# Optimization experiments

Hardware: AMD Instinct MI355X
Metric: run time of the kernel (lower is better)

The kernel has to match this reference:

```python
import jax, jax.numpy as jnp
import numpy as np

THETA0 = 3.0
THETA = 5.0
BIG = 1e10  # stands in for +inf in the squared-distance transform


def _edt_sq_1d(f):
    # f: [..., n] of squared distances; returns min_j (i-j)^2 + f[j] per i.
    n = f.shape[-1]
    i = jnp.arange(n, dtype=f.dtype)
    d2 = (i[:, None] - i[None, :]) ** 2  # [n, n]
    return jnp.min(f[..., None, :] + d2, axis=-1)


def _edt(mask):
    # Exact Euclidean distance from each voxel to the nearest zero of `mask`
    # (matches scipy.ndimage.distance_transform_edt on a binary mask),
    # via the separable squared-distance transform applied axis by axis.
    f = jnp.where(mask > 0.5, jnp.asarray(BIG, mask.dtype), jnp.asarray(0.0, mask.dtype))
    for ax in range(1, mask.ndim):  # skip batch axis 0
        f = jnp.moveaxis(_edt_sq_1d(jnp.moveaxis(f, ax, -1)), -1, ax)
    return jnp.sqrt(f)


def setup_inputs() -> dict:
    key = jax.random.key(0)
    k1, k2 = jax.random.split(key)
    B, D, H, W = 2, 64, 96, 96
    pred = jax.random.uniform(k1, (B, D, H, W), dtype=jnp.float32)  # probabilities
    target = jax.random.randint(k2, (B, D, H, W), 0, 2).astype(jnp.float32)  # binary mask
    return {"pred": pred, "target": target}


def reference(pred, target):
    # Signed distance phi = dist_to_foreground_boundary framework: 
    # dist_pos = EDT(target) (distance to nearest background voxel),
    # dist_neg = EDT(1 - target).
    dist_pos = _edt(target)
    dist_neg = _edt(1.0 - target)
    a = jnp.abs(dist_neg - dist_pos)
    w = jnp.where(
        a <= THETA0,
        1.0,
        jnp.where(a >= THETA, 0.0, 1.0 - (a - THETA0) / (THETA - THETA0)),
    )
    w = jax.lax.stop_gradient(w)  # original computes weights from detached numpy target

    # binary_cross_entropy with torch's log clamp at -100
    log_p = jnp.clip(jnp.log(pred), -100.0)
    log_1mp = jnp.clip(jnp.log(1.0 - pred), -100.0)
    bce = -(target * log_p + (1.0 - target) * log_1mp)  # [B, D, H, W]

    num = jnp.sum(bce * w, axis=(1, 2, 3))
    den = jnp.sum(w, axis=(1, 2, 3)) + 1e-5
    return jnp.mean(num / den)
```

## Files before the change

### kernel.cpp

```cpp
#include <hip/hip_runtime.h>
#include <math.h>

#define BDIM 2
#define DDIM 64
#define HDIM 96
#define WDIM 96
#define HW   (HDIM * WDIM)
#define DHW  (DDIM * HW)

#define DT 16
#define DH 24
#define HT 8
#define HH 16
#define WT 32
#define NROWS (DH * HH)
#define NBLK  (BDIM * (DDIM / DT) * (HDIM / HT) * (WDIM / WT))

__global__ void init_acc(float* __restrict__ acc) {
    if (threadIdx.x < 4) acc[threadIdx.x] = 0.0f;
    if (threadIdx.x == 4) ((int*)acc)[4] = 0;
}

__device__ __forceinline__ unsigned nearest2i(unsigned occ) {
    unsigned r = 25u;
    if (occ & 0x101u) r = 16u;
    if (occ & 0x082u) r = 9u;
    if (occ & 0x044u) r = 4u;
    if (occ & 0x028u) r = 1u;
    if (occ & 0x010u) r = 0u;
    return r;
}

__global__ __launch_bounds__(256) void boundary_fused(const float* __restrict__ pred,
                                                      const float* __restrict__ target,
                                                      float* __restrict__ acc,
                                                      float* __restrict__ out) {
    __shared__ unsigned fgb[NROWS * 2];
    __shared__ unsigned vbb[NROWS * 2];
    __shared__ unsigned char swp[DH * HH * WT];
    __shared__ unsigned char swn[DH * HH * WT];
    __shared__ unsigned char whp[DH * HT * WT];
    __shared__ unsigned char whn[DH * HT * WT];
    __shared__ float rsum[8];

    const int tid = threadIdx.x;
    int x = blockIdx.x;
    const int wt = x % 3;  x /= 3;
    const int ht = x % 12; x /= 12;
    const int dt = x % 4;
    const int b  = x / 4;
    const int d0 = dt * DT, h0 = ht * HT, w0 = wt * WT;

    for (int i = tid; i < NROWS * 2; i += 256) { fgb[i] = 0u; vbb[i] = 0u; }
    __syncthreads();

    for (int idx = tid; idx < NROWS * 10; idx += 256) {
        const int row = idx / 10, q = idx - row * 10;
        const int dr = row >> 4, hr = row & 15;
        const int d = d0 - 4 + dr, h = h0 - 4 + hr;
        if (d < 0 || d >= DDIM || h < 0 || h >= HDIM) continue;
        const int wbase = w0 - 4 + q * 4;
        const float* rowp = target + ((size_t)(b * DDIM + d) * HDIM + h) * WDIM;
        unsigned fgn = 0u, vn = 0u;
        if (wbase >= 0 && wbase <= WDIM - 4) {
            float4 v4 = *(const float4*)(rowp + wbase);
            fgn = (unsigned)(v4.x > 0.5f) | ((unsigned)(v4.y > 0.5f) << 1) |
                  ((unsigned)(v4.z > 0.5f) << 2) | ((unsigned)(v4.w > 0.5f) << 3);
            vn = 0xFu;
        } else {
            for (int j = 0; j < 4; ++j) {
                int w = wbase + j;
                if (w >= 0 && w < WDIM) {
                    vn |= 1u << j;
                    if (rowp[w] > 0.5f) fgn |= 1u << j;
                }
            }
        }
        if (vn) {
            const int k = q * 4, word = k >> 5, sh = k & 31;
            if (fgn) atomicOr(&fgb[row * 2 + word], fgn << sh);
            atomicOr(&vbb[row * 2 + word], vn << sh);
        }
    }
    __syncthreads();

    for (int idx = tid; idx < NROWS * WT; idx += 256) {
        const int row = idx >> 5, wi = idx & 31;
        unsigned long long fg = ((unsigned long long)fgb[row * 2 + 1] << 32) | fgb[row * 2];
        unsigned long long vv = ((unsigned long long)vbb[row * 2 + 1] << 32) | vbb[row * 2];
        unsigned of = (unsigned)(fg >> wi) & 0x1FFu;
        unsigned ov = (unsigned)(vv >> wi) & 0x1FFu;
        unsigned ob = ~of & ov;
        swn[idx] = (unsigned char)nearest2i(of);
        swp[idx] = (unsigned char)nearest2i(ob);
    }
    __syncthreads();

    for (int idx = tid; idx < DH * HT * WT; idx += 256) {
        const int dr = idx >> 8;
        const int hh = (idx >> 5) & 7;
        const int wi = idx & 31;
        unsigned p = 25u, n = 25u;
        #pragma unroll
        for (int t = 0; t < 9; ++t) {
            const unsigned d2 = (unsigned)((t - 4) * (t - 4));
            const int src = (dr * HH + hh + t) * WT + wi;
            p = min(p, d2 + (unsigned)swp[src]);
            n = min(n, d2 + (unsigned)swn[src]);
        }
        whp[idx] = (unsigned char)p;
        whn[idx] = (unsigned char)n;
    }
    __syncthreads();

    float num = 0.f, den = 0.f;
    #pragma unroll 4
    for (int it = 0; it < 16; ++it) {
        const int idx = tid + 256 * it;
        const int di = idx >> 8;
        const int hh = (idx >> 5) & 7;
        const int wi = idx & 31;
        unsigned p = 25u, n = 25u;
        #pragma unroll
        for (int t = 0; t < 9; ++t) {
            const unsigned d2 = (unsigned)((t - 4) * (t - 4));
            const int src = ((di + t) * HT + hh) * WT + wi;
            p = min(p, d2 + (unsigned)whp[src]);
            n = min(n, d2 + (unsigned)whn[src]);
        }
        const size_t g = ((size_t)(b * DDIM + d0 + di) * HDIM + h0 + hh) * WDIM + w0 + wi;
        const float pr = pred[g];
        const float tg = target[g];
        const float dp = sqrtf((float)p);
        const float dn = sqrtf((float)n);
        const float a  = fabsf(dn - dp);
        float w;
        if (a <= 3.0f)      w = 1.0f;
        else if (a >= 5.0f) w = 0.0f;
        else                w = 1.0f - (a - 3.0f) * 0.5f;
        const float lp  = fmaxf(logf(pr), -100.0f);
        const float l1  = fmaxf(logf(1.0f - pr), -100.0f);
        const float bce = -(tg * lp + (1.0f - tg) * l1);
        num += bce * w;
        den += w;
    }

    for (int off = 32; off > 0; off >>= 1) {
        num += __shfl_down(num, off);
        den += __shfl_down(den, off);
    }
    if ((tid & 63) == 0) {
        rsum[tid >> 6]       = num;
        rsum[4 + (tid >> 6)] = den;
    }
    __syncthreads();
    if (tid == 0) {
        float ns = rsum[0] + rsum[1] + rsum[2] + rsum[3];
        float ds = rsum[4] + rsum[5] + rsum[6] + rsum[7];
        atomicAdd(&acc[b], ns);
        atomicAdd(&acc[2 + b], ds);
        __threadfence();
        int done = atomicAdd((int*)acc + 4, 1);
        if (done == NBLK - 1) {
            __threadfence();
            float n0 = atomicAdd(&acc[0], 0.0f);
            float n1 = atomicAdd(&acc[1], 0.0f);
            float d0_ = atomicAdd(&acc[2], 0.0f);
            float d1_ = atomicAdd(&acc[3], 0.0f);
            out[0] = 0.5f * (n0 / (d0_ + 1e-5f) + n1 / (d1_ + 1e-5f));
        }
    }
}

extern "C" void kernel_launch(void* const* d_in, const int* in_sizes, int n_in,
                              void* d_out, int out_size, void* d_ws, size_t ws_size,
                              hipStream_t stream) {
    const float* pred   = (const float*)d_in[0];
    const float* target = (const float*)d_in[1];
    float* acc = (float*)d_ws;
    float* out = (float*)d_out;

    init_acc<<<1, 64, 0, stream>>>(acc);
    boundary_fused<<<NBLK, 256, 0, stream>>>(pred, target, acc, out);
}
```

Before: 95.13 us.

## Pack EDT distances four per word with SWAR min and ballot-based bitmask build

Halves the depth tile to 8 so each block holds 16 halo rows, which doubles the number of blocks. Foreground bitmasks are built with a wave ballot over 40 lanes instead of shared atomicOr. Squared distances for four voxels are packed as bytes in one 32-bit word, and the H and D passes use a SWAR byte-wise min, which cuts shared-memory traffic and ALU work. The final stage loads pred and target as float4. The smaller depth tile raises the halo overhead ratio from 24/16 to 16/8, and the byte packing depends on every value staying below 128.

```diff
diff --git a/kernel.cpp b/kernel.cpp
--- a/kernel.cpp
+++ b/kernel.cpp
@@ -8,11 +8,11 @@
 #define HW   (HDIM * WDIM)
 #define DHW  (DDIM * HW)
 
-#define DT 16
-#define DH 24
+#define DT 8
 #define HT 8
+#define WT 32
+#define DH 16
 #define HH 16
-#define WT 32
 #define NROWS (DH * HH)
 #define NBLK  (BDIM * (DDIM / DT) * (HDIM / HT) * (WDIM / WT))
 
@@ -31,118 +31,139 @@
     return r;
 }
 
+__device__ __forceinline__ unsigned vminu4(unsigned a, unsigned b) {
+    unsigned c = ((a | 0x80808080u) - b) & 0x80808080u;
+    unsigned m = (c - (c >> 7)) | c;
+    return a ^ ((a ^ b) & m);
+}
+
 __global__ __launch_bounds__(256) void boundary_fused(const float* __restrict__ pred,
                                                       const float* __restrict__ target,
                                                       float* __restrict__ acc,
                                                       float* __restrict__ out) {
-    __shared__ unsigned fgb[NROWS * 2];
-    __shared__ unsigned vbb[NROWS * 2];
-    __shared__ unsigned char swp[DH * HH * WT];
-    __shared__ unsigned char swn[DH * HH * WT];
-    __shared__ unsigned char whp[DH * HT * WT];
-    __shared__ unsigned char whn[DH * HT * WT];
+    __shared__ unsigned long long fgb[NROWS];
+    __shared__ unsigned swp[NROWS * 8];
+    __shared__ unsigned swn[NROWS * 8];
+    __shared__ unsigned whp[DH * HT * 8];
+    __shared__ unsigned whn[DH * HT * 8];
     __shared__ float rsum[8];
 
     const int tid = threadIdx.x;
     int x = blockIdx.x;
     const int wt = x % 3;  x /= 3;
     const int ht = x % 12; x /= 12;
-    const int dt = x % 4;
-    const int b  = x / 4;
+    const int dt = x % 8;
+    const int b  = x / 8;
     const int d0 = dt * DT, h0 = ht * HT, w0 = wt * WT;
 
-    for (int i = tid; i < NROWS * 2; i += 256) { fgb[i] = 0u; vbb[i] = 0u; }
-    __syncthreads();
-
-    for (int idx = tid; idx < NROWS * 10; idx += 256) {
-        const int row = idx / 10, q = idx - row * 10;
-        const int dr = row >> 4, hr = row & 15;
-        const int d = d0 - 4 + dr, h = h0 - 4 + hr;
-        if (d < 0 || d >= DDIM || h < 0 || h >= HDIM) continue;
-        const int wbase = w0 - 4 + q * 4;
-        const float* rowp = target + ((size_t)(b * DDIM + d) * HDIM + h) * WDIM;
-        unsigned fgn = 0u, vn = 0u;
-        if (wbase >= 0 && wbase <= WDIM - 4) {
-            float4 v4 = *(const float4*)(rowp + wbase);
-            fgn = (unsigned)(v4.x > 0.5f) | ((unsigned)(v4.y > 0.5f) << 1) |
-                  ((unsigned)(v4.z > 0.5f) << 2) | ((unsigned)(v4.w > 0.5f) << 3);
-            vn = 0xFu;
-        } else {
+    unsigned long long vb_row = (1ULL << 40) - 1;
+    if (wt == 0) vb_row &= ~0xFULL;
+    if (wt == 2) vb_row &= (1ULL << 36) - 1;
+
+    {
+        const int lane = tid & 63;
+        const int wv   = tid >> 6;
+        #pragma unroll 4
+        for (int i = 0; i < 64; ++i) {
+            const int row = wv * 64 + i;
+            const int dr = row >> 4, hr = row & 15;
+            const int d = d0 - 4 + dr, h = h0 - 4 + hr, w = w0 - 4 + lane;
+            const bool valid = (lane < 40) && ((unsigned)d < DDIM) &&
+                               ((unsigned)h < HDIM) && ((unsigned)w < WDIM);
+            float v = 0.0f;
+            if (valid) v = target[((size_t)(b * DDIM + d) * HDIM + h) * WDIM + w];
+            unsigned long long bb = __ballot(v > 0.5f);
+            if (lane == 0) fgb[row] = bb;
+        }
+    }
+    __syncthreads();
+
+    {
+        const int q  = tid & 7;
+        const int rg = tid >> 3;
+        #pragma unroll
+        for (int k = 0; k < 8; ++k) {
+            const int row = rg + 32 * k;
+            const int dr = row >> 4, hr = row & 15;
+            const bool rv = ((unsigned)(d0 - 4 + dr) < DDIM) &&
+                            ((unsigned)(h0 - 4 + hr) < HDIM);
+            const unsigned long long fg = fgb[row];
+            const unsigned long long vb = rv ? vb_row : 0ULL;
+            unsigned pa = 0u, na = 0u;
+            #pragma unroll
             for (int j = 0; j < 4; ++j) {
-                int w = wbase + j;
-                if (w >= 0 && w < WDIM) {
-                    vn |= 1u << j;
-                    if (rowp[w] > 0.5f) fgn |= 1u << j;
-                }
+                const int wi = q * 4 + j;
+                const unsigned of = (unsigned)(fg >> wi) & 0x1FFu;
+                const unsigned ov = (unsigned)(vb >> wi) & 0x1FFu;
+                const unsigned ob = ~of & ov;
+                na |= nearest2i(of) << (8 * j);
+                pa |= nearest2i(ob) << (8 * j);
             }
-        }
-        if (vn) {
-            const int k = q * 4, word = k >> 5, sh = k & 31;
-            if (fgn) atomicOr(&fgb[row * 2 + word], fgn << sh);
-            atomicOr(&vbb[row * 2 + word], vn << sh);
-        }
-    }
-    __syncthreads();
-
-    for (int idx = tid; idx < NROWS * WT; idx += 256) {
-        const int row = idx >> 5, wi = idx & 31;
-        unsigned long long fg = ((unsigned long long)fgb[row * 2 + 1] << 32) | fgb[row * 2];
-        unsigned long long vv = ((unsigned long long)vbb[row * 2 + 1] << 32) | vbb[row * 2];
-        unsigned of = (unsigned)(fg >> wi) & 0x1FFu;
-        unsigned ov = (unsigned)(vv >> wi) & 0x1FFu;
-        unsigned ob = ~of & ov;
-        swn[idx] = (unsigned char)nearest2i(of);
-        swp[idx] = (unsigned char)nearest2i(ob);
-    }
-    __syncthreads();
-
-    for (int idx = tid; idx < DH * HT * WT; idx += 256) {
-        const int dr = idx >> 8;
-        const int hh = (idx >> 5) & 7;
-        const int wi = idx & 31;
-        unsigned p = 25u, n = 25u;
+            swp[row * 8 + q] = pa;
+            swn[row * 8 + q] = na;
+        }
+    }
+    __syncthreads();
+
+    #pragma unroll
+    for (int k = 0; k < 4; ++k) {
+        const int g  = tid + 256 * k;
+        const int q  = g & 7;
+        const int hh = (g >> 3) & 7;
+        const int dr = g >> 6;
+        unsigned p = 0x19191919u, n = 0x19191919u;
         #pragma unroll
         for (int t = 0; t < 9; ++t) {
-            const unsigned d2 = (unsigned)((t - 4) * (t - 4));
-            const int src = (dr * HH + hh + t) * WT + wi;
-            p = min(p, d2 + (unsigned)swp[src]);
-            n = min(n, d2 + (unsigned)swn[src]);
-        }
-        whp[idx] = (unsigned char)p;
-        whn[idx] = (unsigned char)n;
+            const int dd = (t - 4) * (t - 4);
+            const unsigned add = (unsigned)dd * 0x01010101u;
+            const int src = (dr * HH + hh + t) * 8 + q;
+            p = vminu4(p, swp[src] + add);
+            n = vminu4(n, swn[src] + add);
+        }
+        whp[(dr * HT + hh) * 8 + q] = p;
+        whn[(dr * HT + hh) * 8 + q] = n;
     }
     __syncthreads();
 
     float num = 0.f, den = 0.f;
-    #pragma unroll 4
-    for (int it = 0; it < 16; ++it) {
-        const int idx = tid + 256 * it;
-        const int di = idx >> 8;
-        const int hh = (idx >> 5) & 7;
-        const int wi = idx & 31;
-        unsigned p = 25u, n = 25u;
+    #pragma unroll
+    for (int k = 0; k < 2; ++k) {
+        const int g  = tid + 256 * k;
+        const int q  = g & 7;
+        const int hh = (g >> 3) & 7;
+        const int di = g >> 6;
+        unsigned p = 0x19191919u, n = 0x19191919u;
         #pragma unroll
         for (int t = 0; t < 9; ++t) {
-            const unsigned d2 = (unsigned)((t - 4) * (t - 4));
-            const int src = ((di + t) * HT + hh) * WT + wi;
-            p = min(p, d2 + (unsigned)whp[src]);
-            n = min(n, d2 + (unsigned)whn[src]);
-        }
-        const size_t g = ((size_t)(b * DDIM + d0 + di) * HDIM + h0 + hh) * WDIM + w0 + wi;
-        const float pr = pred[g];
-        const float tg = target[g];
-        const float dp = sqrtf((float)p);
-        const float dn = sqrtf((float)n);
-        const float a  = fabsf(dn - dp);
-        float w;
-        if (a <= 3.0f)      w = 1.0f;
-        else if (a >= 5.0f) w = 0.0f;
-        else                w = 1.0f - (a - 3.0f) * 0.5f;
-        const float lp  = fmaxf(logf(pr), -100.0f);
-        const float l1  = fmaxf(logf(1.0f - pr), -100.0f);
-        const float bce = -(tg * lp + (1.0f - tg) * l1);
-        num += bce * w;
-        den += w;
+            const int dd = (t - 4) * (t - 4);
+            const unsigned add = (unsigned)dd * 0x01010101u;
+            const int src = ((di + t) * HT + hh) * 8 + q;
+            p = vminu4(p, whp[src] + add);
+            n = vminu4(n, whn[src] + add);
+        }
+        const size_t gg = ((size_t)(b * DDIM + d0 + di) * HDIM + h0 + hh) * WDIM
+                        + w0 + q * 4;
+        const float4 pr = *(const float4*)(pred + gg);
+        const float4 tg = *(const float4*)(target + gg);
+        #pragma unroll
+        for (int j = 0; j < 4; ++j) {
+            const float pv = (float)((p >> (8 * j)) & 0xFFu);
+            const float nv = (float)((n >> (8 * j)) & 0xFFu);
+            const float prj = j == 0 ? pr.x : j == 1 ? pr.y : j == 2 ? pr.z : pr.w;
+            const float tgj = j == 0 ? tg.x : j == 1 ? tg.y : j == 2 ? tg.z : tg.w;
+            const float dp = sqrtf(pv);
+            const float dn = sqrtf(nv);
+            const float a  = fabsf(dn - dp);
+            float w;
+            if (a <= 3.0f)      w = 1.0f;
+            else if (a >= 5.0f) w = 0.0f;
+            else                w = 1.0f - (a - 3.0f) * 0.5f;
+            const float lp  = fmaxf(logf(prj), -100.0f);
+            const float l1  = fmaxf(logf(1.0f - prj), -100.0f);
+            const float bce = -(tgj * lp + (1.0f - tgj) * l1);
+            num += bce * w;
+            den += w;
+        }
     }
 
     for (int off = 32; off > 0; off >>= 1) {
@@ -163,8 +184,8 @@
         int done = atomicAdd((int*)acc + 4, 1);
         if (done == NBLK - 1) {
             __threadfence();
-            float n0 = atomicAdd(&acc[0], 0.0f);
-            float n1 = atomicAdd(&acc[1], 0.0f);
+            float n0  = atomicAdd(&acc[0], 0.0f);
+            float n1  = atomicAdd(&acc[1], 0.0f);
             float d0_ = atomicAdd(&acc[2], 0.0f);
             float d1_ = atomicAdd(&acc[3], 0.0f);
             out[0] = 0.5f * (n0 / (d0_ + 1e-5f) + n1 / (d1_ + 1e-5f));
```

After: 109.3 us. 14.9% more time.
